# Kernel optimization log

Measured on AMD Instinct MI355X. Metric: run time of the kernel, lower is better.

Reference implementation:

```python
import jax, jax.numpy as jnp
import numpy as np

N = 50000      # nodes
E = 200000     # edges per edge type (avg in-degree 16 over 4 etypes)
R = 4          # number of edge types
DIN = 128
DH = 128
DOUT = 64


def setup_inputs() -> dict:
    key = jax.random.key(0)
    ks = jax.random.split(key, 6)
    feat = jax.random.normal(ks[0], (N, DIN), dtype=jnp.float32)
    edges = jax.random.randint(ks[1], (R, 2, E), 0, N)  # [R, (src,dst), E]
    s1 = 1.0 / np.sqrt(DIN)
    W1 = jax.random.uniform(ks[2], (R, DIN, DH), jnp.float32, -s1, s1)
    b1 = jax.random.uniform(ks[3], (R, DH), jnp.float32, -s1, s1)
    s2 = 1.0 / np.sqrt(DH)
    W2 = jax.random.uniform(ks[4], (R, DH, DOUT), jnp.float32, -s2, s2)
    b2 = jax.random.uniform(ks[5], (R, DOUT), jnp.float32, -s2, s2)
    return {"feat": feat, "W1": W1, "b1": b1, "W2": W2, "b2": b2, "edges": edges}


def _hetero_layer(h, W, b, edges):
    """Per-etype Linear -> copy_u + mean over in-edges -> sum across etypes."""
    n = h.shape[0]

    def per_etype(Wr, br, er):
        Wh = h @ Wr + br                       # [N, d_out]
        src, dst = er[0], er[1]
        msg = Wh[src]                          # gather [E, d_out]
        ssum = jax.ops.segment_sum(msg, dst, num_segments=n)
        deg = jax.ops.segment_sum(jnp.ones((er.shape[1],), Wh.dtype), dst,
                                  num_segments=n)
        return ssum / jnp.maximum(deg, 1.0)[:, None]   # mean; 0 for isolated nodes

    return jax.vmap(per_etype)(W, b, edges).sum(axis=0)  # 'sum' cross reducer


def reference(feat, W1, b1, W2, b2, edges):
    h = _hetero_layer(feat, W1, b1, edges)
    h = jax.nn.relu(h)
    return _hetero_layer(h, W2, b2, edges)
```

## Files before the change

### kernel.cpp

```cpp
#include <hip/hip_runtime.h>

#define NN 50000
#define EE 200000
#define RR 4
#define SC_TOTAL (RR * NN)
#define CAP 32
#define GTILE ((NN + 127) / 128)
#define NB_G1 (4 * GTILE)
#define NB_F  1563

typedef __attribute__((ext_vector_type(8))) short bf16x8;
typedef __attribute__((ext_vector_type(4))) float f32x4;

__device__ inline unsigned short f2bf(float x) {
    unsigned int u = __float_as_uint(x);
    u += 0x7fffu + ((u >> 16) & 1u);
    return (unsigned short)(u >> 16);
}
__device__ inline float bflo(unsigned u) { return __uint_as_float(u << 16); }
__device__ inline float bfhi(unsigned u) { return __uint_as_float(u & 0xffff0000u); }

__device__ inline bf16x8 pk8(float4 x, float4 y) {
    bf16x8 o;
    o[0] = (short)f2bf(x.x); o[1] = (short)f2bf(x.y);
    o[2] = (short)f2bf(x.z); o[3] = (short)f2bf(x.w);
    o[4] = (short)f2bf(y.x); o[5] = (short)f2bf(y.y);
    o[6] = (short)f2bf(y.z); o[7] = (short)f2bf(y.w);
    return o;
}

__global__ __launch_bounds__(256) void init_kernel(
    const float* __restrict__ W1, const float* __restrict__ b1,
    const float* __restrict__ W2, const float* __restrict__ b2,
    unsigned short* __restrict__ W1T, unsigned short* __restrict__ W2T,
    float* __restrict__ btab1, float* __restrict__ btab2,
    int* __restrict__ cnt)
{
    int b = blockIdx.x, t = threadIdx.x;
    if (b < 256) {
        int i = b * 256 + t;
        int jout = i >> 7, k = i & 127;
        int r = jout >> 7, j = jout & 127;
        W1T[i] = f2bf(W1[r * 16384 + k * 128 + j]);
    } else if (b < 384) {
        int i = (b - 256) * 256 + t;
        int jout = i >> 7, k = i & 127;
        int r = jout >> 6, j = jout & 63;
        W2T[i] = f2bf(W2[r * 8192 + k * 64 + j]);
    } else if (b < 392) {
        int i = (b - 384) * 256 + t;
        int mm = i >> 7, c = i & 127;
        float s = 0.f;
        #pragma unroll
        for (int r = 0; r < RR; ++r) if (mm & (1 << r)) s += b1[r * 128 + c];
        btab1[i] = s;
    } else if (b < 396) {
        int i = (b - 392) * 256 + t;
        int mm = i >> 6, c = i & 63;
        float s = 0.f;
        #pragma unroll
        for (int r = 0; r < RR; ++r) if (mm & (1 << r)) s += b2[r * 64 + c];
        btab2[i] = s;
    } else {
        int i = ((b - 396) * 256 + t) * 4;
        if (i < SC_TOTAL) *(int4*)&cnt[i] = make_int4(0, 0, 0, 0);
    }
}

__global__ __launch_bounds__(256) void fill_gemm1(
    const int* __restrict__ edges, int* __restrict__ cnt,
    unsigned short* __restrict__ ssrc2,
    const float* __restrict__ feat, const unsigned short* __restrict__ WT,
    unsigned short* __restrict__ H)
{
    __shared__ __align__(16) unsigned short Wl[128 * 128];
    const int bid = blockIdx.x;
    const int tid = threadIdx.x;

    if (bid & 1) {
        int f = bid >> 1;
        #pragma unroll
        for (int k = 0; k < 2; ++k) {
            int i = f * 512 + k * 256 + tid;
            if (i < RR * EE) {
                int r = i / EE;
                int e = i - r * EE;
                const int* es = edges + (size_t)r * 2 * EE;
                int src = es[e];
                int dst = es[EE + e];
                int seg = r * NN + dst;
                int p = atomicAdd(&cnt[seg], 1);
                if (p < CAP) ssrc2[(size_t)seg * CAP + p] = (unsigned short)src;
            }
        }
        return;
    }

    const int g    = bid >> 1;
    const int wv   = tid >> 6;
    const int lane = tid & 63;
    const int m    = lane & 15;
    const int q    = lane >> 4;
    const int col0 = (g & 3) * 128;
    const int row0 = (g >> 2) * 128;

    #pragma unroll
    for (int i = 0; i < 8; ++i) {
        int L  = i * 4096 + tid * 16;
        int nr = L >> 8, ir = L & 255;
        uint4 v = *(const uint4*)((const char*)WT + ((size_t)(col0 + nr) << 8) + ir);
        *(uint4*)((char*)Wl + nr * 256 + (ir ^ ((nr & 7) << 4))) = v;
    }
    __syncthreads();

    f32x4 acc[2][8];
    #pragma unroll
    for (int rf = 0; rf < 2; ++rf)
        #pragma unroll
        for (int nt = 0; nt < 8; ++nt) acc[rf][nt] = (f32x4){0.f, 0.f, 0.f, 0.f};

    const int ra0 = row0 + wv * 32 + m;
    const int ra1 = ra0 + 16;
    const bool g0 = ra0 < NN, g1 = ra1 < NN;
    const float* Af0 = feat + (size_t)ra0 * 128 + q * 8;
    const float* Af1 = feat + (size_t)ra1 * 128 + q * 8;
    const bf16x8 bz = (bf16x8){0, 0, 0, 0, 0, 0, 0, 0};

    #pragma unroll
    for (int kk = 0; kk < 4; ++kk) {
        bf16x8 a0 = bz, a1 = bz;
        if (g0) {
            float4 x = *(const float4*)(Af0 + kk * 32);
            float4 y = *(const float4*)(Af0 + kk * 32 + 4);
            a0 = pk8(x, y);
        }
        if (g1) {
            float4 x = *(const float4*)(Af1 + kk * 32);
            float4 y = *(const float4*)(Af1 + kk * 32 + 4);
            a1 = pk8(x, y);
        }
        #pragma unroll
        for (int nt = 0; nt < 8; ++nt) {
            int offb = (nt * 16 + m) * 256 + ((kk * 64 + q * 16) ^ ((m & 7) << 4));
            bf16x8 bfr = *(const bf16x8*)((const char*)Wl + offb);
            acc[0][nt] = __builtin_amdgcn_mfma_f32_16x16x32_bf16(a0, bfr, acc[0][nt], 0, 0, 0);
            acc[1][nt] = __builtin_amdgcn_mfma_f32_16x16x32_bf16(a1, bfr, acc[1][nt], 0, 0, 0);
        }
    }

    #pragma unroll
    for (int rf = 0; rf < 2; ++rf) {
        #pragma unroll
        for (int rg = 0; rg < 4; ++rg) {
            int row = row0 + wv * 32 + rf * 16 + q * 4 + rg;
            if (row < NN) {
                unsigned short* Hp = H + (size_t)row * 512 + col0 + m;
                #pragma unroll
                for (int nt = 0; nt < 8; ++nt)
                    Hp[nt * 16] = f2bf(acc[rf][nt][rg]);
            }
        }
    }
}

template<int OTOT>
__global__ __launch_bounds__(256) void gemm_tf(
    const unsigned short* __restrict__ A, const unsigned short* __restrict__ WT,
    unsigned short* __restrict__ H)
{
    __shared__ __align__(16) unsigned short Wl[128 * 128];
    const int tid  = threadIdx.x;
    const int wv   = tid >> 6;
    const int lane = tid & 63;
    const int m    = lane & 15;
    const int q    = lane >> 4;
    const int col0 = blockIdx.x * 128;
    const int row0 = blockIdx.y * 128;

    #pragma unroll
    for (int i = 0; i < 8; ++i) {
        int L  = i * 4096 + tid * 16;
        int nr = L >> 8, ir = L & 255;
        uint4 v = *(const uint4*)((const char*)WT + ((size_t)(col0 + nr) << 8) + ir);
        *(uint4*)((char*)Wl + nr * 256 + (ir ^ ((nr & 7) << 4))) = v;
    }
    __syncthreads();

    f32x4 acc[2][8];
    #pragma unroll
    for (int rf = 0; rf < 2; ++rf)
        #pragma unroll
        for (int nt = 0; nt < 8; ++nt) acc[rf][nt] = (f32x4){0.f, 0.f, 0.f, 0.f};

    const int ra0 = row0 + wv * 32 + m;
    const int ra1 = ra0 + 16;
    const bool g0 = ra0 < NN, g1 = ra1 < NN;
    const unsigned short* Ap0 = A + (size_t)ra0 * 128 + q * 8;
    const unsigned short* Ap1 = A + (size_t)ra1 * 128 + q * 8;
    const bf16x8 bz = (bf16x8){0, 0, 0, 0, 0, 0, 0, 0};

    #pragma unroll
    for (int kk = 0; kk < 4; ++kk) {
        bf16x8 a0 = g0 ? *(const bf16x8*)(Ap0 + kk * 32) : bz;
        bf16x8 a1 = g1 ? *(const bf16x8*)(Ap1 + kk * 32) : bz;
        #pragma unroll
        for (int nt = 0; nt < 8; ++nt) {
            int offb = (nt * 16 + m) * 256 + ((kk * 64 + q * 16) ^ ((m & 7) << 4));
            bf16x8 bfr = *(const bf16x8*)((const char*)Wl + offb);
            acc[0][nt] = __builtin_amdgcn_mfma_f32_16x16x32_bf16(a0, bfr, acc[0][nt], 0, 0, 0);
            acc[1][nt] = __builtin_amdgcn_mfma_f32_16x16x32_bf16(a1, bfr, acc[1][nt], 0, 0, 0);
        }
    }

    #pragma unroll
    for (int rf = 0; rf < 2; ++rf) {
        #pragma unroll
        for (int rg = 0; rg < 4; ++rg) {
            int row = row0 + wv * 32 + rf * 16 + q * 4 + rg;
            if (row < NN) {
                unsigned short* Hp = H + (size_t)row * OTOT + col0 + m;
                #pragma unroll
                for (int nt = 0; nt < 8; ++nt)
                    Hp[nt * 16] = f2bf(acc[rf][nt][rg]);
            }
        }
    }
}

__global__ __launch_bounds__(256) void gather_node1(
    const unsigned short* __restrict__ H1, const unsigned short* __restrict__ ssrc2,
    const int* __restrict__ cnt, const float* __restrict__ btab1,
    unsigned short* __restrict__ h1r)
{
    int n = blockIdx.x * 16 + (threadIdx.x >> 4);
    if (n >= NN) return;
    int l = threadIdx.x & 15;

    int   dg[RR];
    uint4 id[RR];
    #pragma unroll
    for (int r = 0; r < RR; ++r) {
        int seg = r * NN + n;
        dg[r] = cnt[seg];
        id[r] = *(const uint4*)(ssrc2 + (size_t)seg * CAP);
    }

    float ac[RR][8];
    #pragma unroll
    for (int r = 0; r < RR; ++r)
        #pragma unroll
        for (int i = 0; i < 8; ++i) ac[r][i] = 0.f;

    #pragma unroll
    for (int j = 0; j < 8; ++j) {
        #pragma unroll
        for (int r = 0; r < RR; ++r) {
            if (j < dg[r]) {
                unsigned w = (j >> 1) == 0 ? id[r].x : (j >> 1) == 1 ? id[r].y
                           : (j >> 1) == 2 ? id[r].z : id[r].w;
                unsigned s = (j & 1) ? (w >> 16) : (w & 0xffffu);
                uint4 u = *(const uint4*)(H1 + r * 128 + l * 8 + (size_t)s * 512);
                ac[r][0] += bflo(u.x); ac[r][1] += bfhi(u.x);
                ac[r][2] += bflo(u.y); ac[r][3] += bfhi(u.y);
                ac[r][4] += bflo(u.z); ac[r][5] += bfhi(u.z);
                ac[r][6] += bflo(u.w); ac[r][7] += bfhi(u.w);
            }
        }
    }
    if ((dg[0] | dg[1] | dg[2] | dg[3]) > 8) {
        #pragma unroll
        for (int r = 0; r < RR; ++r) {
            int nd = dg[r] < CAP ? dg[r] : CAP;
            for (int j = 8; j < nd; ++j) {
                unsigned s = ssrc2[(size_t)(r * NN + n) * CAP + j];
                uint4 u = *(const uint4*)(H1 + r * 128 + l * 8 + (size_t)s * 512);
                ac[r][0] += bflo(u.x); ac[r][1] += bfhi(u.x);
                ac[r][2] += bflo(u.y); ac[r][3] += bfhi(u.y);
                ac[r][4] += bflo(u.z); ac[r][5] += bfhi(u.z);
                ac[r][6] += bflo(u.w); ac[r][7] += bfhi(u.w);
            }
        }
    }

    int mk = (dg[0] > 0 ? 1 : 0) | (dg[1] > 0 ? 2 : 0) |
             (dg[2] > 0 ? 4 : 0) | (dg[3] > 0 ? 8 : 0);
    float iv[RR];
    #pragma unroll
    for (int r = 0; r < RR; ++r) iv[r] = dg[r] > 0 ? 1.0f / (float)dg[r] : 0.f;

    const float* bt = btab1 + mk * 128 + l * 8;
    float4 t0 = *(const float4*)bt;
    float4 t1 = *(const float4*)(bt + 4);
    float o0[8] = {t0.x, t0.y, t0.z, t0.w, t1.x, t1.y, t1.z, t1.w};
    #pragma unroll
    for (int i = 0; i < 8; ++i) {
        #pragma unroll
        for (int r = 0; r < RR; ++r) o0[i] += ac[r][i] * iv[r];
        o0[i] = fmaxf(o0[i], 0.f);
    }
    uint4 o;
    o.x = (unsigned)f2bf(o0[0]) | ((unsigned)f2bf(o0[1]) << 16);
    o.y = (unsigned)f2bf(o0[2]) | ((unsigned)f2bf(o0[3]) << 16);
    o.z = (unsigned)f2bf(o0[4]) | ((unsigned)f2bf(o0[5]) << 16);
    o.w = (unsigned)f2bf(o0[6]) | ((unsigned)f2bf(o0[7]) << 16);
    *(uint4*)&h1r[(size_t)n * 128 + l * 8] = o;
}

__global__ __launch_bounds__(256) void gather_node2(
    const unsigned short* __restrict__ H2, const unsigned short* __restrict__ ssrc2,
    const int* __restrict__ cnt, const float* __restrict__ btab2,
    float* __restrict__ out)
{
    int n = blockIdx.x * 32 + (threadIdx.x >> 3);
    if (n >= NN) return;
    int l = threadIdx.x & 7;

    int   dg[RR];
    uint4 id[RR];
    #pragma unroll
    for (int r = 0; r < RR; ++r) {
        int seg = r * NN + n;
        dg[r] = cnt[seg];
        id[r] = *(const uint4*)(ssrc2 + (size_t)seg * CAP);
    }

    float ac[RR][8];
    #pragma unroll
    for (int r = 0; r < RR; ++r)
        #pragma unroll
        for (int i = 0; i < 8; ++i) ac[r][i] = 0.f;

    #pragma unroll
    for (int j = 0; j < 8; ++j) {
        #pragma unroll
        for (int r = 0; r < RR; ++r) {
            if (j < dg[r]) {
                unsigned w = (j >> 1) == 0 ? id[r].x : (j >> 1) == 1 ? id[r].y
                           : (j >> 1) == 2 ? id[r].z : id[r].w;
                unsigned s = (j & 1) ? (w >> 16) : (w & 0xffffu);
                uint4 u = *(const uint4*)(H2 + r * 64 + l * 8 + (size_t)s * 256);
                ac[r][0] += bflo(u.x); ac[r][1] += bfhi(u.x);
                ac[r][2] += bflo(u.y); ac[r][3] += bfhi(u.y);
                ac[r][4] += bflo(u.z); ac[r][5] += bfhi(u.z);
                ac[r][6] += bflo(u.w); ac[r][7] += bfhi(u.w);
            }
        }
    }
    if ((dg[0] | dg[1] | dg[2] | dg[3]) > 8) {
        #pragma unroll
        for (int r = 0; r < RR; ++r) {
            int nd = dg[r] < CAP ? dg[r] : CAP;
            for (int j = 8; j < nd; ++j) {
                unsigned s = ssrc2[(size_t)(r * NN + n) * CAP + j];
                uint4 u = *(const uint4*)(H2 + r * 64 + l * 8 + (size_t)s * 256);
                ac[r][0] += bflo(u.x); ac[r][1] += bfhi(u.x);
                ac[r][2] += bflo(u.y); ac[r][3] += bfhi(u.y);
                ac[r][4] += bflo(u.z); ac[r][5] += bfhi(u.z);
                ac[r][6] += bflo(u.w); ac[r][7] += bfhi(u.w);
            }
        }
    }

    int mk = (dg[0] > 0 ? 1 : 0) | (dg[1] > 0 ? 2 : 0) |
             (dg[2] > 0 ? 4 : 0) | (dg[3] > 0 ? 8 : 0);
    float iv[RR];
    #pragma unroll
    for (int r = 0; r < RR; ++r) iv[r] = dg[r] > 0 ? 1.0f / (float)dg[r] : 0.f;

    const float* bt = btab2 + mk * 64 + l * 8;
    float4 t0 = *(const float4*)bt;
    float4 t1 = *(const float4*)(bt + 4);
    float o0[8] = {t0.x, t0.y, t0.z, t0.w, t1.x, t1.y, t1.z, t1.w};
    #pragma unroll
    for (int i = 0; i < 8; ++i)
        #pragma unroll
        for (int r = 0; r < RR; ++r) o0[i] += ac[r][i] * iv[r];

    float* op = out + (size_t)n * 64 + l * 8;
    *(float4*)op       = make_float4(o0[0], o0[1], o0[2], o0[3]);
    *(float4*)(op + 4) = make_float4(o0[4], o0[5], o0[6], o0[7]);
}

extern "C" void kernel_launch(void* const* d_in, const int* in_sizes, int n_in,
                              void* d_out, int out_size, void* d_ws, size_t ws_size,
                              hipStream_t stream)
{
    const float* feat  = (const float*)d_in[0];
    const float* W1    = (const float*)d_in[1];
    const float* b1    = (const float*)d_in[2];
    const float* W2    = (const float*)d_in[3];
    const float* b2    = (const float*)d_in[4];
    const int*   edges = (const int*)d_in[5];
    float* out = (float*)d_out;

    char* p = (char*)d_ws;
    auto alloc = [&](size_t bytes) { char* q = p; p += (bytes + 255) & ~(size_t)255; return q; };
    int* cnt                 = (int*)alloc((size_t)SC_TOTAL * 4);
    unsigned short* ssrc2    = (unsigned short*)alloc((size_t)SC_TOTAL * CAP * 2);
    unsigned short* W1T      = (unsigned short*)alloc((size_t)512 * 128 * 2);
    unsigned short* W2T      = (unsigned short*)alloc((size_t)256 * 128 * 2);
    float* btab1             = (float*)alloc((size_t)16 * 128 * 4);
    float* btab2             = (float*)alloc((size_t)16 * 64 * 4);
    unsigned short* h1r      = (unsigned short*)alloc((size_t)NN * 128 * 2);
    unsigned short* H        = (unsigned short*)alloc((size_t)NN * 512 * 2);

    init_kernel<<<592, 256, 0, stream>>>(W1, b1, W2, b2,
                                         W1T, W2T, btab1, btab2, cnt);
    fill_gemm1<<<NB_G1 + NB_F, 256, 0, stream>>>(edges, cnt, ssrc2, feat, W1T, H);
    gather_node1<<<(NN + 15) / 16, 256, 0, stream>>>(H, ssrc2, cnt, btab1, h1r);
    gemm_tf<256><<<dim3(2, GTILE), 256, 0, stream>>>(h1r, W2T, H);
    gather_node2<<<(NN + 31) / 32, 256, 0, stream>>>(H, ssrc2, cnt, btab2, out);
}
```

Before: 220.5 us.

## Fuse layer-1 gather with layer-2 GEMM and pre-convert feat to bf16

Merges the layer-1 neighbor-mean gather, bias and ReLU with the layer-2 MFMA GEMM into one kernel, so the h1r intermediate is never written or re-read and one launch goes away. Each lane now gathers 32 features per neighbor and reads W2T straight from global memory instead of LDS. The feat-to-bf16 conversion moves into init_kernel, which makes fill_gemm1's GEMM read bf16, but adds an extra pass over feat. The fused kernel carries much higher register pressure and uncoalesced per-row gathers, which risks lower occupancy.

New measurement: 231.2 us. +4.8%, slower.

```diff
diff --git a/kernel.cpp b/kernel.cpp
--- a/kernel.cpp
+++ b/kernel.cpp
@@ -20,16 +20,8 @@
 __device__ inline float bflo(unsigned u) { return __uint_as_float(u << 16); }
 __device__ inline float bfhi(unsigned u) { return __uint_as_float(u & 0xffff0000u); }
 
-__device__ inline bf16x8 pk8(float4 x, float4 y) {
-    bf16x8 o;
-    o[0] = (short)f2bf(x.x); o[1] = (short)f2bf(x.y);
-    o[2] = (short)f2bf(x.z); o[3] = (short)f2bf(x.w);
-    o[4] = (short)f2bf(y.x); o[5] = (short)f2bf(y.y);
-    o[6] = (short)f2bf(y.z); o[7] = (short)f2bf(y.w);
-    return o;
-}
-
 __global__ __launch_bounds__(256) void init_kernel(
+    const float* __restrict__ feat, unsigned short* __restrict__ featb,
     const float* __restrict__ W1, const float* __restrict__ b1,
     const float* __restrict__ W2, const float* __restrict__ b2,
     unsigned short* __restrict__ W1T, unsigned short* __restrict__ W2T,
@@ -37,32 +29,38 @@
     int* __restrict__ cnt)
 {
     int b = blockIdx.x, t = threadIdx.x;
-    if (b < 256) {
-        int i = b * 256 + t;
+    if (b < 6250) {
+        int i = (b * 256 + t) * 4;
+        float4 v = *(const float4*)&feat[i];
+        unsigned lo = (unsigned)f2bf(v.x) | ((unsigned)f2bf(v.y) << 16);
+        unsigned hi = (unsigned)f2bf(v.z) | ((unsigned)f2bf(v.w) << 16);
+        *(uint2*)&featb[i] = make_uint2(lo, hi);
+    } else if (b < 6506) {
+        int i = (b - 6250) * 256 + t;
         int jout = i >> 7, k = i & 127;
         int r = jout >> 7, j = jout & 127;
         W1T[i] = f2bf(W1[r * 16384 + k * 128 + j]);
-    } else if (b < 384) {
-        int i = (b - 256) * 256 + t;
+    } else if (b < 6634) {
+        int i = (b - 6506) * 256 + t;
         int jout = i >> 7, k = i & 127;
         int r = jout >> 6, j = jout & 63;
         W2T[i] = f2bf(W2[r * 8192 + k * 64 + j]);
-    } else if (b < 392) {
-        int i = (b - 384) * 256 + t;
+    } else if (b < 6642) {
+        int i = (b - 6634) * 256 + t;
         int mm = i >> 7, c = i & 127;
         float s = 0.f;
         #pragma unroll
         for (int r = 0; r < RR; ++r) if (mm & (1 << r)) s += b1[r * 128 + c];
         btab1[i] = s;
-    } else if (b < 396) {
-        int i = (b - 392) * 256 + t;
+    } else if (b < 6646) {
+        int i = (b - 6642) * 256 + t;
         int mm = i >> 6, c = i & 63;
         float s = 0.f;
         #pragma unroll
         for (int r = 0; r < RR; ++r) if (mm & (1 << r)) s += b2[r * 64 + c];
         btab2[i] = s;
     } else {
-        int i = ((b - 396) * 256 + t) * 4;
+        int i = ((b - 6646) * 256 + t) * 4;
         if (i < SC_TOTAL) *(int4*)&cnt[i] = make_int4(0, 0, 0, 0);
     }
 }
@@ -70,7 +68,7 @@
 __global__ __launch_bounds__(256) void fill_gemm1(
     const int* __restrict__ edges, int* __restrict__ cnt,
     unsigned short* __restrict__ ssrc2,
-    const float* __restrict__ feat, const unsigned short* __restrict__ WT,
+    const unsigned short* __restrict__ A, const unsigned short* __restrict__ WT,
     unsigned short* __restrict__ H)
 {
     __shared__ __align__(16) unsigned short Wl[128 * 128];
@@ -122,23 +120,14 @@
     const int ra0 = row0 + wv * 32 + m;
     const int ra1 = ra0 + 16;
     const bool g0 = ra0 < NN, g1 = ra1 < NN;
-    const float* Af0 = feat + (size_t)ra0 * 128 + q * 8;
-    const float* Af1 = feat + (size_t)ra1 * 128 + q * 8;
+    const unsigned short* Ap0 = A + (size_t)ra0 * 128 + q * 8;
+    const unsigned short* Ap1 = A + (size_t)ra1 * 128 + q * 8;
     const bf16x8 bz = (bf16x8){0, 0, 0, 0, 0, 0, 0, 0};
 
     #pragma unroll
     for (int kk = 0; kk < 4; ++kk) {
-        bf16x8 a0 = bz, a1 = bz;
-        if (g0) {
-            float4 x = *(const float4*)(Af0 + kk * 32);
-            float4 y = *(const float4*)(Af0 + kk * 32 + 4);
-            a0 = pk8(x, y);
-        }
-        if (g1) {
-            float4 x = *(const float4*)(Af1 + kk * 32);
-            float4 y = *(const float4*)(Af1 + kk * 32 + 4);
-            a1 = pk8(x, y);
-        }
+        bf16x8 a0 = g0 ? *(const bf16x8*)(Ap0 + kk * 32) : bz;
+        bf16x8 a1 = g1 ? *(const bf16x8*)(Ap1 + kk * 32) : bz;
         #pragma unroll
         for (int nt = 0; nt < 8; ++nt) {
             int offb = (nt * 16 + m) * 256 + ((kk * 64 + q * 16) ^ ((m & 7) << 4));
@@ -163,147 +152,117 @@
     }
 }
 
-template<int OTOT>
-__global__ __launch_bounds__(256) void gemm_tf(
-    const unsigned short* __restrict__ A, const unsigned short* __restrict__ WT,
-    unsigned short* __restrict__ H)
-{
-    __shared__ __align__(16) unsigned short Wl[128 * 128];
+__global__ __launch_bounds__(256) void gather_gemm2(
+    const unsigned short* __restrict__ H1, const unsigned short* __restrict__ ssrc2,
+    const int* __restrict__ cnt, const float* __restrict__ btab1,
+    const unsigned short* __restrict__ W2T, unsigned short* __restrict__ H2)
+{
     const int tid  = threadIdx.x;
     const int wv   = tid >> 6;
     const int lane = tid & 63;
     const int m    = lane & 15;
     const int q    = lane >> 4;
-    const int col0 = blockIdx.x * 128;
-    const int row0 = blockIdx.y * 128;
-
-    #pragma unroll
-    for (int i = 0; i < 8; ++i) {
-        int L  = i * 4096 + tid * 16;
-        int nr = L >> 8, ir = L & 255;
-        uint4 v = *(const uint4*)((const char*)WT + ((size_t)(col0 + nr) << 8) + ir);
-        *(uint4*)((char*)Wl + nr * 256 + (ir ^ ((nr & 7) << 4))) = v;
-    }
-    __syncthreads();
-
-    f32x4 acc[2][8];
-    #pragma unroll
-    for (int rf = 0; rf < 2; ++rf)
-        #pragma unroll
-        for (int nt = 0; nt < 8; ++nt) acc[rf][nt] = (f32x4){0.f, 0.f, 0.f, 0.f};
-
-    const int ra0 = row0 + wv * 32 + m;
-    const int ra1 = ra0 + 16;
-    const bool g0 = ra0 < NN, g1 = ra1 < NN;
-    const unsigned short* Ap0 = A + (size_t)ra0 * 128 + q * 8;
-    const unsigned short* Ap1 = A + (size_t)ra1 * 128 + q * 8;
-    const bf16x8 bz = (bf16x8){0, 0, 0, 0, 0, 0, 0, 0};
-
+    const int n0   = blockIdx.x * 64;
+    const int n    = n0 + wv * 16 + m;
+
+    float tot[32];
+    #pragma unroll
+    for (int i = 0; i < 32; ++i) tot[i] = 0.f;
+    int mk = 0;
+
+    if (n < NN) {
+        int   dg[RR];
+        uint4 id[RR];
+        #pragma unroll
+        for (int r = 0; r < RR; ++r) {
+            int seg = r * NN + n;
+            dg[r] = cnt[seg];
+            id[r] = *(const uint4*)(ssrc2 + (size_t)seg * CAP);
+        }
+        #pragma unroll
+        for (int r = 0; r < RR; ++r) {
+            if (dg[r] > 0) {
+                mk |= 1 << r;
+                int nd = dg[r] < CAP ? dg[r] : CAP;
+                float tmp[32];
+                #pragma unroll
+                for (int i = 0; i < 32; ++i) tmp[i] = 0.f;
+                #pragma unroll
+                for (int j = 0; j < 8; ++j) {
+                    if (j < nd) {
+                        unsigned w = (j >> 1) == 0 ? id[r].x : (j >> 1) == 1 ? id[r].y
+                                   : (j >> 1) == 2 ? id[r].z : id[r].w;
+                        unsigned s = (j & 1) ? (w >> 16) : (w & 0xffffu);
+                        const unsigned short* row = H1 + (size_t)s * 512 + r * 128 + q * 8;
+                        #pragma unroll
+                        for (int kk = 0; kk < 4; ++kk) {
+                            uint4 u = *(const uint4*)(row + kk * 32);
+                            tmp[kk*8+0] += bflo(u.x); tmp[kk*8+1] += bfhi(u.x);
+                            tmp[kk*8+2] += bflo(u.y); tmp[kk*8+3] += bfhi(u.y);
+                            tmp[kk*8+4] += bflo(u.z); tmp[kk*8+5] += bfhi(u.z);
+                            tmp[kk*8+6] += bflo(u.w); tmp[kk*8+7] += bfhi(u.w);
+                        }
+                    }
+                }
+                for (int j = 8; j < nd; ++j) {
+                    unsigned s = ssrc2[(size_t)(r * NN + n) * CAP + j];
+                    const unsigned short* row = H1 + (size_t)s * 512 + r * 128 + q * 8;
+                    #pragma unroll
+                    for (int kk = 0; kk < 4; ++kk) {
+                        uint4 u = *(const uint4*)(row + kk * 32);
+                        tmp[kk*8+0] += bflo(u.x); tmp[kk*8+1] += bfhi(u.x);
+                        tmp[kk*8+2] += bflo(u.y); tmp[kk*8+3] += bfhi(u.y);
+                        tmp[kk*8+4] += bflo(u.z); tmp[kk*8+5] += bfhi(u.z);
+                        tmp[kk*8+6] += bflo(u.w); tmp[kk*8+7] += bfhi(u.w);
+                    }
+                }
+                float iv = 1.0f / (float)dg[r];
+                #pragma unroll
+                for (int i = 0; i < 32; ++i) tot[i] += tmp[i] * iv;
+            }
+        }
+    }
+
+    const float* bt = btab1 + mk * 128 + q * 8;
+    bf16x8 af[4];
     #pragma unroll
     for (int kk = 0; kk < 4; ++kk) {
-        bf16x8 a0 = g0 ? *(const bf16x8*)(Ap0 + kk * 32) : bz;
-        bf16x8 a1 = g1 ? *(const bf16x8*)(Ap1 + kk * 32) : bz;
-        #pragma unroll
-        for (int nt = 0; nt < 8; ++nt) {
-            int offb = (nt * 16 + m) * 256 + ((kk * 64 + q * 16) ^ ((m & 7) << 4));
-            bf16x8 bfr = *(const bf16x8*)((const char*)Wl + offb);
-            acc[0][nt] = __builtin_amdgcn_mfma_f32_16x16x32_bf16(a0, bfr, acc[0][nt], 0, 0, 0);
-            acc[1][nt] = __builtin_amdgcn_mfma_f32_16x16x32_bf16(a1, bfr, acc[1][nt], 0, 0, 0);
-        }
-    }
-
-    #pragma unroll
-    for (int rf = 0; rf < 2; ++rf) {
-        #pragma unroll
-        for (int rg = 0; rg < 4; ++rg) {
-            int row = row0 + wv * 32 + rf * 16 + q * 4 + rg;
-            if (row < NN) {
-                unsigned short* Hp = H + (size_t)row * OTOT + col0 + m;
-                #pragma unroll
-                for (int nt = 0; nt < 8; ++nt)
-                    Hp[nt * 16] = f2bf(acc[rf][nt][rg]);
-            }
-        }
-    }
-}
-
-__global__ __launch_bounds__(256) void gather_node1(
-    const unsigned short* __restrict__ H1, const unsigned short* __restrict__ ssrc2,
-    const int* __restrict__ cnt, const float* __restrict__ btab1,
-    unsigned short* __restrict__ h1r)
-{
-    int n = blockIdx.x * 16 + (threadIdx.x >> 4);
-    if (n >= NN) return;
-    int l = threadIdx.x & 15;
-
-    int   dg[RR];
-    uint4 id[RR];
-    #pragma unroll
-    for (int r = 0; r < RR; ++r) {
-        int seg = r * NN + n;
-        dg[r] = cnt[seg];
-        id[r] = *(const uint4*)(ssrc2 + (size_t)seg * CAP);
-    }
-
-    float ac[RR][8];
-    #pragma unroll
-    for (int r = 0; r < RR; ++r)
-        #pragma unroll
-        for (int i = 0; i < 8; ++i) ac[r][i] = 0.f;
-
-    #pragma unroll
-    for (int j = 0; j < 8; ++j) {
-        #pragma unroll
-        for (int r = 0; r < RR; ++r) {
-            if (j < dg[r]) {
-                unsigned w = (j >> 1) == 0 ? id[r].x : (j >> 1) == 1 ? id[r].y
-                           : (j >> 1) == 2 ? id[r].z : id[r].w;
-                unsigned s = (j & 1) ? (w >> 16) : (w & 0xffffu);
-                uint4 u = *(const uint4*)(H1 + r * 128 + l * 8 + (size_t)s * 512);
-                ac[r][0] += bflo(u.x); ac[r][1] += bfhi(u.x);
-                ac[r][2] += bflo(u.y); ac[r][3] += bfhi(u.y);
-                ac[r][4] += bflo(u.z); ac[r][5] += bfhi(u.z);
-                ac[r][6] += bflo(u.w); ac[r][7] += bfhi(u.w);
-            }
-        }
-    }
-    if ((dg[0] | dg[1] | dg[2] | dg[3]) > 8) {
-        #pragma unroll
-        for (int r = 0; r < RR; ++r) {
-            int nd = dg[r] < CAP ? dg[r] : CAP;
-            for (int j = 8; j < nd; ++j) {
-                unsigned s = ssrc2[(size_t)(r * NN + n) * CAP + j];
-                uint4 u = *(const uint4*)(H1 + r * 128 + l * 8 + (size_t)s * 512);
-                ac[r][0] += bflo(u.x); ac[r][1] += bfhi(u.x);
-                ac[r][2] += bflo(u.y); ac[r][3] += bfhi(u.y);
-                ac[r][4] += bflo(u.z); ac[r][5] += bfhi(u.z);
-                ac[r][6] += bflo(u.w); ac[r][7] += bfhi(u.w);
-            }
-        }
-    }
-
-    int mk = (dg[0] > 0 ? 1 : 0) | (dg[1] > 0 ? 2 : 0) |
-             (dg[2] > 0 ? 4 : 0) | (dg[3] > 0 ? 8 : 0);
-    float iv[RR];
-    #pragma unroll
-    for (int r = 0; r < RR; ++r) iv[r] = dg[r] > 0 ? 1.0f / (float)dg[r] : 0.f;
-
-    const float* bt = btab1 + mk * 128 + l * 8;
-    float4 t0 = *(const float4*)bt;
-    float4 t1 = *(const float4*)(bt + 4);
-    float o0[8] = {t0.x, t0.y, t0.z, t0.w, t1.x, t1.y, t1.z, t1.w};
-    #pragma unroll
-    for (int i = 0; i < 8; ++i) {
-        #pragma unroll
-        for (int r = 0; r < RR; ++r) o0[i] += ac[r][i] * iv[r];
-        o0[i] = fmaxf(o0[i], 0.f);
-    }
-    uint4 o;
-    o.x = (unsigned)f2bf(o0[0]) | ((unsigned)f2bf(o0[1]) << 16);
-    o.y = (unsigned)f2bf(o0[2]) | ((unsigned)f2bf(o0[3]) << 16);
-    o.z = (unsigned)f2bf(o0[4]) | ((unsigned)f2bf(o0[5]) << 16);
-    o.w = (unsigned)f2bf(o0[6]) | ((unsigned)f2bf(o0[7]) << 16);
-    *(uint4*)&h1r[(size_t)n * 128 + l * 8] = o;
+        float4 t0 = *(const float4*)(bt + kk * 32);
+        float4 t1 = *(const float4*)(bt + kk * 32 + 4);
+        bf16x8 a;
+        a[0] = (short)f2bf(fmaxf(tot[kk*8+0] + t0.x, 0.f));
+        a[1] = (short)f2bf(fmaxf(tot[kk*8+1] + t0.y, 0.f));
+        a[2] = (short)f2bf(fmaxf(tot[kk*8+2] + t0.z, 0.f));
+        a[3] = (short)f2bf(fmaxf(tot[kk*8+3] + t0.w, 0.f));
+        a[4] = (short)f2bf(fmaxf(tot[kk*8+4] + t1.x, 0.f));
+        a[5] = (short)f2bf(fmaxf(tot[kk*8+5] + t1.y, 0.f));
+        a[6] = (short)f2bf(fmaxf(tot[kk*8+6] + t1.z, 0.f));
+        a[7] = (short)f2bf(fmaxf(tot[kk*8+7] + t1.w, 0.f));
+        af[kk] = a;
+    }
+
+    f32x4 acc[16];
+    #pragma unroll
+    for (int nt = 0; nt < 16; ++nt) acc[nt] = (f32x4){0.f, 0.f, 0.f, 0.f};
+    #pragma unroll
+    for (int kk = 0; kk < 4; ++kk) {
+        #pragma unroll
+        for (int nt = 0; nt < 16; ++nt) {
+            bf16x8 bfr = *(const bf16x8*)(W2T + (size_t)(nt * 16 + m) * 128 + kk * 32 + q * 8);
+            acc[nt] = __builtin_amdgcn_mfma_f32_16x16x32_bf16(af[kk], bfr, acc[nt], 0, 0, 0);
+        }
+    }
+
+    #pragma unroll
+    for (int rg = 0; rg < 4; ++rg) {
+        int row = n0 + wv * 16 + q * 4 + rg;
+        if (row < NN) {
+            unsigned short* Hp = H2 + (size_t)row * 256 + m;
+            #pragma unroll
+            for (int nt = 0; nt < 16; ++nt)
+                Hp[nt * 16] = f2bf(acc[nt][rg]);
+        }
+    }
 }
 
 __global__ __launch_bounds__(256) void gather_node2(
@@ -401,13 +360,13 @@
     unsigned short* W2T      = (unsigned short*)alloc((size_t)256 * 128 * 2);
     float* btab1             = (float*)alloc((size_t)16 * 128 * 4);
     float* btab2             = (float*)alloc((size_t)16 * 64 * 4);
-    unsigned short* h1r      = (unsigned short*)alloc((size_t)NN * 128 * 2);
+    unsigned short* featb    = (unsigned short*)alloc((size_t)NN * 128 * 2);
     unsigned short* H        = (unsigned short*)alloc((size_t)NN * 512 * 2);
-
-    init_kernel<<<592, 256, 0, stream>>>(W1, b1, W2, b2,
-                                         W1T, W2T, btab1, btab2, cnt);
-    fill_gemm1<<<NB_G1 + NB_F, 256, 0, stream>>>(edges, cnt, ssrc2, feat, W1T, H);
-    gather_node1<<<(NN + 15) / 16, 256, 0, stream>>>(H, ssrc2, cnt, btab1, h1r);
-    gemm_tf<256><<<dim3(2, GTILE), 256, 0, stream>>>(h1r, W2T, H);
-    gather_node2<<<(NN + 31) / 32, 256, 0, stream>>>(H, ssrc2, cnt, btab2, out);
-}
+    unsigned short* H2       = (unsigned short*)alloc((size_t)NN * 256 * 2);
+
+    init_kernel<<<6842, 256, 0, stream>>>(feat, featb, W1, b1, W2, b2,
+                                          W1T, W2T, btab1, btab2, cnt);
+    fill_gemm1<<<NB_G1 + NB_F, 256, 0, stream>>>(edges, cnt, ssrc2, featb, W1T, H);
+    gather_gemm2<<<(NN + 63) / 64, 256, 0, stream>>>(H, ssrc2, cnt, btab1, W2T, H2);
+    gather_node2<<<(NN + 31) / 32, 256, 0, stream>>>(H2, ssrc2, cnt, btab2, out);
+}
```

## Stage feat rows once in LDS and compute all GEMM1 column tiles per block

Applied to the files above, without the earlier changes.

GEMM1 blocks now convert a 128-row feat tile to bf16 into swizzled LDS once, then loop over all four 128-column output groups. Previously feat was reloaded and converted four times, once per column tile. Weight fragments are now read directly from global/L2 instead of LDS. Block interleaving with the edge-fill work is rebalanced to 1 GEMM per 4 fill blocks.

Measured after the change: 235.1 us. 6.6% more time.

```diff
diff --git a/kernel.cpp b/kernel.cpp
--- a/kernel.cpp
+++ b/kernel.cpp
@@ -6,8 +6,8 @@
 #define SC_TOTAL (RR * NN)
 #define CAP 32
 #define GTILE ((NN + 127) / 128)
-#define NB_G1 (4 * GTILE)
 #define NB_F  1563
+#define NB_TOT (GTILE + NB_F)
 
 typedef __attribute__((ext_vector_type(8))) short bf16x8;
 typedef __attribute__((ext_vector_type(4))) float f32x4;
@@ -17,17 +17,11 @@
     u += 0x7fffu + ((u >> 16) & 1u);
     return (unsigned short)(u >> 16);
 }
+__device__ inline unsigned pk2(float a, float b) {
+    return (unsigned)f2bf(a) | ((unsigned)f2bf(b) << 16);
+}
 __device__ inline float bflo(unsigned u) { return __uint_as_float(u << 16); }
 __device__ inline float bfhi(unsigned u) { return __uint_as_float(u & 0xffff0000u); }
-
-__device__ inline bf16x8 pk8(float4 x, float4 y) {
-    bf16x8 o;
-    o[0] = (short)f2bf(x.x); o[1] = (short)f2bf(x.y);
-    o[2] = (short)f2bf(x.z); o[3] = (short)f2bf(x.w);
-    o[4] = (short)f2bf(y.x); o[5] = (short)f2bf(y.y);
-    o[6] = (short)f2bf(y.z); o[7] = (short)f2bf(y.w);
-    return o;
-}
 
 __global__ __launch_bounds__(256) void init_kernel(
     const float* __restrict__ W1, const float* __restrict__ b1,
@@ -73,12 +67,12 @@
     const float* __restrict__ feat, const unsigned short* __restrict__ WT,
     unsigned short* __restrict__ H)
 {
-    __shared__ __align__(16) unsigned short Wl[128 * 128];
+    __shared__ __align__(16) unsigned short Al[128 * 128];
     const int bid = blockIdx.x;
     const int tid = threadIdx.x;
 
-    if (bid & 1) {
-        int f = bid >> 1;
+    if (bid % 5 != 0) {
+        int f = bid - bid / 5 - 1;
         #pragma unroll
         for (int k = 0; k < 2; ++k) {
             int i = f * 512 + k * 256 + tid;
@@ -96,68 +90,78 @@
         return;
     }
 
-    const int g    = bid >> 1;
+    const int g    = bid / 5;
     const int wv   = tid >> 6;
     const int lane = tid & 63;
     const int m    = lane & 15;
     const int q    = lane >> 4;
-    const int col0 = (g & 3) * 128;
-    const int row0 = (g >> 2) * 128;
-
-    #pragma unroll
-    for (int i = 0; i < 8; ++i) {
-        int L  = i * 4096 + tid * 16;
-        int nr = L >> 8, ir = L & 255;
-        uint4 v = *(const uint4*)((const char*)WT + ((size_t)(col0 + nr) << 8) + ir);
-        *(uint4*)((char*)Wl + nr * 256 + (ir ^ ((nr & 7) << 4))) = v;
+    const int row0 = g * 128;
+
+    #pragma unroll
+    for (int it = 0; it < 4; ++it) {
+        int i  = it * 256 + tid;
+        int rr = i >> 3, c16 = (i & 7) * 16;
+        int row = row0 + rr;
+        uint4 u01 = make_uint4(0, 0, 0, 0), u23 = make_uint4(0, 0, 0, 0);
+        if (row < NN) {
+            const float* fp = feat + (size_t)row * 128 + c16;
+            float4 v0 = *(const float4*)(fp);
+            float4 v1 = *(const float4*)(fp + 4);
+            float4 v2 = *(const float4*)(fp + 8);
+            float4 v3 = *(const float4*)(fp + 12);
+            u01 = make_uint4(pk2(v0.x, v0.y), pk2(v0.z, v0.w),
+                             pk2(v1.x, v1.y), pk2(v1.z, v1.w));
+            u23 = make_uint4(pk2(v2.x, v2.y), pk2(v2.z, v2.w),
+                             pk2(v3.x, v3.y), pk2(v3.z, v3.w));
+        }
+        int base = rr * 256 + c16 * 2;
+        int sw   = (rr & 7) << 4;
+        *(uint4*)((char*)Al + ((base) ^ sw))      = u01;
+        *(uint4*)((char*)Al + ((base + 16) ^ sw)) = u23;
     }
     __syncthreads();
 
-    f32x4 acc[2][8];
-    #pragma unroll
-    for (int rf = 0; rf < 2; ++rf)
-        #pragma unroll
-        for (int nt = 0; nt < 8; ++nt) acc[rf][nt] = (f32x4){0.f, 0.f, 0.f, 0.f};
-
-    const int ra0 = row0 + wv * 32 + m;
-    const int ra1 = ra0 + 16;
-    const bool g0 = ra0 < NN, g1 = ra1 < NN;
-    const float* Af0 = feat + (size_t)ra0 * 128 + q * 8;
-    const float* Af1 = feat + (size_t)ra1 * 128 + q * 8;
-    const bf16x8 bz = (bf16x8){0, 0, 0, 0, 0, 0, 0, 0};
-
-    #pragma unroll
-    for (int kk = 0; kk < 4; ++kk) {
-        bf16x8 a0 = bz, a1 = bz;
-        if (g0) {
-            float4 x = *(const float4*)(Af0 + kk * 32);
-            float4 y = *(const float4*)(Af0 + kk * 32 + 4);
-            a0 = pk8(x, y);
-        }
-        if (g1) {
-            float4 x = *(const float4*)(Af1 + kk * 32);
-            float4 y = *(const float4*)(Af1 + kk * 32 + 4);
-            a1 = pk8(x, y);
-        }
-        #pragma unroll
-        for (int nt = 0; nt < 8; ++nt) {
-            int offb = (nt * 16 + m) * 256 + ((kk * 64 + q * 16) ^ ((m & 7) << 4));
-            bf16x8 bfr = *(const bf16x8*)((const char*)Wl + offb);
-            acc[0][nt] = __builtin_amdgcn_mfma_f32_16x16x32_bf16(a0, bfr, acc[0][nt], 0, 0, 0);
-            acc[1][nt] = __builtin_amdgcn_mfma_f32_16x16x32_bf16(a1, bfr, acc[1][nt], 0, 0, 0);
-        }
-    }
-
+    bf16x8 af[2][4];
     #pragma unroll
     for (int rf = 0; rf < 2; ++rf) {
-        #pragma unroll
-        for (int rg = 0; rg < 4; ++rg) {
-            int row = row0 + wv * 32 + rf * 16 + q * 4 + rg;
-            if (row < NN) {
-                unsigned short* Hp = H + (size_t)row * 512 + col0 + m;
-                #pragma unroll
-                for (int nt = 0; nt < 8; ++nt)
-                    Hp[nt * 16] = f2bf(acc[rf][nt][rg]);
+        int row = wv * 32 + rf * 16 + m;
+        int sw  = (row & 7) << 4;
+        #pragma unroll
+        for (int kk = 0; kk < 4; ++kk)
+            af[rf][kk] = *(const bf16x8*)((const char*)Al +
+                             ((row * 256 + kk * 64 + q * 16) ^ sw));
+    }
+
+    #pragma unroll
+    for (int cp = 0; cp < 4; ++cp) {
+        f32x4 acc[2][8];
+        #pragma unroll
+        for (int rf = 0; rf < 2; ++rf)
+            #pragma unroll
+            for (int nt = 0; nt < 8; ++nt) acc[rf][nt] = (f32x4){0.f, 0.f, 0.f, 0.f};
+
+        #pragma unroll
+        for (int kk = 0; kk < 4; ++kk) {
+            #pragma unroll
+            for (int nt = 0; nt < 8; ++nt) {
+                bf16x8 bfr = *(const bf16x8*)(WT +
+                    (size_t)(cp * 128 + nt * 16 + m) * 128 + kk * 32 + q * 8);
+                acc[0][nt] = __builtin_amdgcn_mfma_f32_16x16x32_bf16(af[0][kk], bfr, acc[0][nt], 0, 0, 0);
+                acc[1][nt] = __builtin_amdgcn_mfma_f32_16x16x32_bf16(af[1][kk], bfr, acc[1][nt], 0, 0, 0);
+            }
+        }
+
+        #pragma unroll
+        for (int rf = 0; rf < 2; ++rf) {
+            #pragma unroll
+            for (int rg = 0; rg < 4; ++rg) {
+                int row = row0 + wv * 32 + rf * 16 + q * 4 + rg;
+                if (row < NN) {
+                    unsigned short* Hp = H + (size_t)row * 512 + cp * 128 + m;
+                    #pragma unroll
+                    for (int nt = 0; nt < 8; ++nt)
+                        Hp[nt * 16] = f2bf(acc[rf][nt][rg]);
+                }
             }
         }
     }
@@ -299,10 +303,10 @@
         o0[i] = fmaxf(o0[i], 0.f);
     }
     uint4 o;
-    o.x = (unsigned)f2bf(o0[0]) | ((unsigned)f2bf(o0[1]) << 16);
-    o.y = (unsigned)f2bf(o0[2]) | ((unsigned)f2bf(o0[3]) << 16);
-    o.z = (unsigned)f2bf(o0[4]) | ((unsigned)f2bf(o0[5]) << 16);
-    o.w = (unsigned)f2bf(o0[6]) | ((unsigned)f2bf(o0[7]) << 16);
+    o.x = pk2(o0[0], o0[1]);
+    o.y = pk2(o0[2], o0[3]);
+    o.z = pk2(o0[4], o0[5]);
+    o.w = pk2(o0[6], o0[7]);
     *(uint4*)&h1r[(size_t)n * 128 + l * 8] = o;
 }
 
@@ -406,7 +410,7 @@
 
     init_kernel<<<592, 256, 0, stream>>>(W1, b1, W2, b2,
                                          W1T, W2T, btab1, btab2, cnt);
-    fill_gemm1<<<NB_G1 + NB_F, 256, 0, stream>>>(edges, cnt, ssrc2, feat, W1T, H);
+    fill_gemm1<<<NB_TOT, 256, 0, stream>>>(edges, cnt, ssrc2, feat, W1T, H);
     gather_node1<<<(NN + 15) / 16, 256, 0, stream>>>(H, ssrc2, cnt, btab1, h1r);
     gemm_tf<256><<<dim3(2, GTILE), 256, 0, stream>>>(h1r, W2T, H);
     gather_node2<<<(NN + 31) / 32, 256, 0, stream>>>(H, ssrc2, cnt, btab2, out);
```
